# Performance work log

Hardware: AMD Instinct MI355X
Metric: run time of the kernel (lower is better)

Reference implementation:

```python
import jax, jax.numpy as jnp
import numpy as np

ROTARY_DIM = 32
THETA = 10000.0

def _rotate_half(t):
    # interleaved pairs: (..., d) -> rotate each (x1, x2) pair to (-x2, x1)
    x = t.reshape(t.shape[:-1] + (-1, 2))
    x1, x2 = x[..., 0], x[..., 1]
    return jnp.stack([-x2, x1], axis=-1).reshape(t.shape)

def _apply_rope(t, offset=0):
    # t: (B, h, T, dh); rotate only the first ROTARY_DIM dims
    T = t.shape[-2]
    inv_freq = 1.0 / (THETA ** (jnp.arange(0, ROTARY_DIM, 2, dtype=jnp.float32) / ROTARY_DIM))
    pos = jnp.arange(T, dtype=jnp.float32) + offset
    freqs = pos[:, None] * inv_freq[None, :]                 # (T, ROTARY_DIM/2)
    freqs = jnp.repeat(freqs, 2, axis=-1)                    # (T, ROTARY_DIM) interleaved
    cos, sin = jnp.cos(freqs), jnp.sin(freqs)
    t_rot, t_pass = t[..., :ROTARY_DIM], t[..., ROTARY_DIM:]
    t_rot = t_rot * cos + _rotate_half(t_rot) * sin
    return jnp.concatenate([t_rot, t_pass], axis=-1)

def setup_inputs() -> dict:
    key = jax.random.key(0)
    k1, k2, k3 = jax.random.split(key, 3)
    B, T, dim = 4, 1024, 1024
    x = jax.random.normal(k1, (B, T, dim), dtype=jnp.float32)
    Wqkv = jax.random.normal(k2, (dim, 3 * dim), dtype=jnp.float32) * (dim ** -0.5)
    Wout = jax.random.normal(k3, (dim, dim), dtype=jnp.float32) * (dim ** -0.5)
    return {"x": x, "Wqkv": Wqkv, "Wout": Wout}

def reference(x, Wqkv, Wout):
    B, T, dim = x.shape
    n_heads = 16
    dh = dim // n_heads
    qkv = x @ Wqkv                                            # (B, T, 3*dim)
    qkv = qkv.reshape(B, T, 3, n_heads, dh)
    qkv = jnp.transpose(qkv, (2, 0, 3, 1, 4))                 # (3, B, h, T, dh)
    q, k, v = qkv[0], qkv[1], qkv[2]
    q = _apply_rope(q, offset=0)
    k = _apply_rope(k, offset=0)
    scale = 1.0 / jnp.sqrt(jnp.asarray(dh, dtype=x.dtype))
    scores = jnp.einsum('bhqd,bhkd->bhqk', q, k) * scale      # (B, h, T, T)
    causal = jnp.tril(jnp.ones((T, T), dtype=bool))
    scores = jnp.where(causal, scores, jnp.asarray(-jnp.inf, dtype=scores.dtype))
    attn = jax.nn.softmax(scores, axis=-1)
    out = jnp.einsum('bhqk,bhkd->bhqd', attn, v)              # (B, h, T, dh)
    out = jnp.transpose(out, (0, 2, 1, 3)).reshape(B, T, dim)
    return out @ Wout
```

## Files before the change

kernel.cpp:

```cpp
#include <hip/hip_runtime.h>
#include <cstdint>
#include <cstddef>

typedef __bf16 bf16;
typedef __bf16 bf16x4 __attribute__((ext_vector_type(4)));
typedef __bf16 bf16x8 __attribute__((ext_vector_type(8)));
typedef float f32x4 __attribute__((ext_vector_type(4)));

#define DEVINL __device__ __forceinline__

static constexpr int Tn   = 1024;
static constexpr int DIM  = 1024;
static constexpr int NH   = 16;
static constexpr int DH   = 64;
static constexpr int QKVN = 3072;

DEVINL void g2l16(const void* g, void* l) {
  __builtin_amdgcn_global_load_lds(
      (const __attribute__((address_space(1))) void*)g,
      (__attribute__((address_space(3))) void*)l, 16, 0, 0);
}


__global__ void k_f32_to_bf16(const float* __restrict__ in, bf16* __restrict__ out, int n4) {
  int i = blockIdx.x * blockDim.x + threadIdx.x;
  if (i >= n4) return;
  float4 v = reinterpret_cast<const float4*>(in)[i];
  bf16 o[4] = {(bf16)v.x, (bf16)v.y, (bf16)v.z, (bf16)v.w};
  reinterpret_cast<uint2*>(out)[i] = *reinterpret_cast<uint2*>(o);
}

__global__ void k_transpose_w(const float* __restrict__ in, bf16* __restrict__ out, int K, int N) {
  __shared__ float tile[32][33];
  int n0 = blockIdx.x * 32, k0 = blockIdx.y * 32;
  int tx = threadIdx.x, ty = threadIdx.y;
#pragma unroll
  for (int j = 0; j < 32; j += 8)
    tile[ty + j][tx] = in[(size_t)(k0 + ty + j) * N + n0 + tx];
  __syncthreads();
#pragma unroll
  for (int j = 0; j < 32; j += 8)
    out[(size_t)(n0 + ty + j) * K + k0 + tx] = (bf16)tile[tx][ty + j];
}

__global__ void k_rope(bf16* __restrict__ qkv) {
  int idx = blockIdx.x * 256 + threadIdx.x;
  int i = idx & 15;
  int h = (idx >> 4) & 15;
  int w = (idx >> 8) & 1;
  int t = (idx >> 9) & 1023;
  int b = idx >> 19;
  float inv = exp2f(-(float)(2 * i) * (13.287712379549449f / 32.0f));
  float ang = (float)t * inv;
  float sn, cs;
  sincosf(ang, &sn, &cs);
  size_t base = ((size_t)(b * Tn + t)) * QKVN + (size_t)w * DIM + h * DH + 2 * i;
  float x1 = (float)qkv[base], x2 = (float)qkv[base + 1];
  qkv[base]     = (bf16)(x1 * cs - x2 * sn);
  qkv[base + 1] = (bf16)(x2 * cs + x1 * sn);
}

__global__ void k_transpose_v(const bf16* __restrict__ qkv, bf16* __restrict__ vt) {
  __shared__ bf16 tile[32][33];
  int t0 = blockIdx.x * 32, d0 = blockIdx.y * 32;
  int bh = blockIdx.z;
  int b = bh >> 4, h = bh & 15;
  int tx = threadIdx.x, ty = threadIdx.y;
#pragma unroll
  for (int j = 0; j < 32; j += 8)
    tile[ty + j][tx] = qkv[((size_t)(b * Tn + t0 + ty + j)) * QKVN + 2 * DIM + h * DH + d0 + tx];
  __syncthreads();
#pragma unroll
  for (int j = 0; j < 32; j += 8)
    vt[((size_t)(bh * DH + d0 + ty + j)) * Tn + t0 + tx] = tile[tx][ty + j];
}

template <bool F32OUT>
__global__ __launch_bounds__(256) void k_gemm_bt(
    const bf16* __restrict__ A, const bf16* __restrict__ Bt,
    void* __restrict__ Cp, int M, int N, int K) {
  __shared__ bf16 As[128 * 64];
  __shared__ bf16 Bs[128 * 64];
  const int tid  = threadIdx.x;
  const int wave = tid >> 6, lane = tid & 63;
  const int lrow = lane & 15, quad = lane >> 4;
  const int m0 = blockIdx.y * 128, n0 = blockIdx.x * 128;
  const int wm = (wave >> 1) * 64, wn = (wave & 1) * 64;

  f32x4 acc[4][4];
#pragma unroll
  for (int mi = 0; mi < 4; mi++)
#pragma unroll
    for (int ni = 0; ni < 4; ni++) acc[mi][ni] = 0.f;

  for (int k0 = 0; k0 < K; k0 += 64) {
    __syncthreads();
#pragma unroll
    for (int i = 0; i < 4; i++) {
      int li = i * 256 + tid;
      int row = li >> 3, c = li & 7;
      int gc = c ^ (row & 7);
      g2l16(A + (size_t)(m0 + row) * K + k0 + gc * 8, As + li * 8);
    }
#pragma unroll
    for (int i = 0; i < 4; i++) {
      int li = i * 256 + tid;
      int row = li >> 3, c = li & 7;
      int gc = c ^ (row & 7);
      g2l16(Bt + (size_t)(n0 + row) * K + k0 + gc * 8, Bs + li * 8);
    }
    __syncthreads();
#pragma unroll
    for (int ki = 0; ki < 2; ki++) {
      bf16x8 af[4], bfr[4];
#pragma unroll
      for (int mi = 0; mi < 4; mi++) {
        int r = wm + mi * 16 + lrow;
        int pc = (ki * 4 + quad) ^ (r & 7);
        af[mi] = *reinterpret_cast<const bf16x8*>(As + r * 64 + pc * 8);
      }
#pragma unroll
      for (int ni = 0; ni < 4; ni++) {
        int r = wn + ni * 16 + lrow;
        int pc = (ki * 4 + quad) ^ (r & 7);
        bfr[ni] = *reinterpret_cast<const bf16x8*>(Bs + r * 64 + pc * 8);
      }
#pragma unroll
      for (int mi = 0; mi < 4; mi++)
#pragma unroll
        for (int ni = 0; ni < 4; ni++)
          acc[mi][ni] = __builtin_amdgcn_mfma_f32_16x16x32_bf16(af[mi], bfr[ni], acc[mi][ni], 0, 0, 0);
    }
  }

#pragma unroll
  for (int mi = 0; mi < 4; mi++)
#pragma unroll
    for (int ni = 0; ni < 4; ni++) {
      int col = n0 + wn + ni * 16 + lrow;
#pragma unroll
      for (int r = 0; r < 4; r++) {
        int row = m0 + wm + mi * 16 + quad * 4 + r;
        float v = acc[mi][ni][r];
        if (F32OUT)
          reinterpret_cast<float*>(Cp)[(size_t)row * N + col] = v;
        else
          reinterpret_cast<bf16*>(Cp)[(size_t)row * N + col] = (bf16)v;
      }
    }
}

__global__ __launch_bounds__(256) void k_attn(
    const bf16* __restrict__ qkv, const bf16* __restrict__ vt,
    bf16* __restrict__ ao) {
  __shared__ bf16 Ks[2][64 * 64];
  __shared__ bf16 Vs[2][64 * 64];
  __shared__ bf16 Ps[8][16 * 64];

  const int tid  = threadIdx.x;
  const int wave = tid >> 6, lane = tid & 63;
  const int lrow = lane & 15, quad = lane >> 4;
  const int bh = blockIdx.y, b = bh >> 4, h = bh & 15;
  const int jn = blockIdx.x;
  const int jf = 15 - jn;
  const int qwf = jf * 64 + wave * 16;
  const int qwn = jn * 64 + wave * 16;
  const size_t qbase = (size_t)b * Tn * QKVN;

  bf16x8 qff[2], qfn[2];
  {
    const float SC = 0.125f * 1.44269504088896f;
    const bf16* qpf = qkv + qbase + (size_t)(qwf + lrow) * QKVN + h * DH;
    const bf16* qpn = qkv + qbase + (size_t)(qwn + lrow) * QKVN + h * DH;
    qff[0] = *reinterpret_cast<const bf16x8*>(qpf + quad * 8);
    qff[1] = *reinterpret_cast<const bf16x8*>(qpf + 32 + quad * 8);
    qfn[0] = *reinterpret_cast<const bf16x8*>(qpn + quad * 8);
    qfn[1] = *reinterpret_cast<const bf16x8*>(qpn + 32 + quad * 8);
#pragma unroll
    for (int j = 0; j < 8; j++) {
      qff[0][j] = (bf16)((float)qff[0][j] * SC);
      qff[1][j] = (bf16)((float)qff[1][j] * SC);
      qfn[0][j] = (bf16)((float)qfn[0][j] * SC);
      qfn[1][j] = (bf16)((float)qfn[1][j] * SC);
    }
  }

  f32x4 oaf[4], oan[4];
#pragma unroll
  for (int g = 0; g < 4; g++) { oaf[g] = 0.f; oan[g] = 0.f; }
  float lif = 0.f, lin = 0.f;

  const int ntiles = jf + 1;

  auto stage = [&](int k0, int bufi) {
#pragma unroll
    for (int i = 0; i < 2; i++) {
      int li2 = i * 256 + tid;
      int row = li2 >> 3, c = li2 & 7;
      int gc = c ^ (row & 7);
      g2l16(qkv + qbase + (size_t)(k0 + row) * QKVN + DIM + h * DH + gc * 8,
            &Ks[bufi][li2 * 8]);
      g2l16(vt + ((size_t)bh * DH + row) * Tn + k0 + gc * 8,
            &Vs[bufi][li2 * 8]);
    }
  };

  auto unit = [&](const bf16* ks, const bf16* vs, bf16x8 (&qf)[2], f32x4 (&oa)[4],
                  float& li, int pi, bool diag) {
    f32x4 s[4];
#pragma unroll
    for (int g = 0; g < 4; g++) s[g] = 0.f;
#pragma unroll
    for (int kh = 0; kh < 2; kh++) {
      const int cX = ((kh * 4 + quad) ^ (lrow & 7)) << 3;
#pragma unroll
      for (int g = 0; g < 4; g++) {
        bf16x8 kf = *reinterpret_cast<const bf16x8*>(ks + (g * 16 + lrow) * 64 + cX);
        s[g] = __builtin_amdgcn_mfma_f32_16x16x32_bf16(kf, qf[kh], s[g], 0, 0, 0);
      }
    }
    float psum = 0.f;
    const int qrel = wave * 16 + lrow;
#pragma unroll
    for (int g = 0; g < 4; g++) {
      bf16x4 pk;
#pragma unroll
      for (int r = 0; r < 4; r++) {
        float p = exp2f(s[g][r]);
        if (diag) {
          int kl = g * 16 + quad * 4 + r;
          p = (kl <= qrel) ? p : 0.f;
        }
        psum += p;
        pk[r] = (bf16)p;
      }
      int chunk = 2 * g + (quad >> 1);
      *reinterpret_cast<bf16x4*>(
          Ps[pi] + lrow * 64 + ((chunk ^ (lrow & 7)) << 3) + 4 * (quad & 1)) = pk;
    }
    li += psum;
#pragma unroll
    for (int kh = 0; kh < 2; kh++) {
      const int cX = ((kh * 4 + quad) ^ (lrow & 7)) << 3;
      bf16x8 pf = *reinterpret_cast<const bf16x8*>(Ps[pi] + lrow * 64 + cX);
#pragma unroll
      for (int g = 0; g < 4; g++) {
        bf16x8 vf = *reinterpret_cast<const bf16x8*>(vs + (g * 16 + lrow) * 64 + cX);
        oa[g] = __builtin_amdgcn_mfma_f32_16x16x32_bf16(pf, vf, oa[g], 0, 0, 0);
      }
    }
  };

  stage(0, 0);

  for (int kt = 0; kt < ntiles; kt++) {
    const int buf = kt & 1;
    __syncthreads();
    if (kt + 1 < ntiles) stage((kt + 1) << 6, buf ^ 1);

    const bf16* ks = Ks[buf];
    const bf16* vs = Vs[buf];

    unit(ks, vs, qff, oaf, lif, wave * 2 + 0, kt == jf);
    if (kt <= jn)
      unit(ks, vs, qfn, oan, lin, wave * 2 + 1, kt == jn);
  }

  lif += __shfl_xor(lif, 16, 64); lif += __shfl_xor(lif, 32, 64);
  lin += __shfl_xor(lin, 16, 64); lin += __shfl_xor(lin, 32, 64);

#pragma unroll
  for (int r = 0; r < 4; r++) {
    int m = quad * 4 + r;
    float invf = 1.0f / __shfl(lif, m, 64);
    float invn = 1.0f / __shfl(lin, m, 64);
    bf16* dstf = ao + ((size_t)b * Tn + qwf + m) * DIM + h * DH;
    bf16* dstn = ao + ((size_t)b * Tn + qwn + m) * DIM + h * DH;
    dstf[ 0 + lrow] = (bf16)(oaf[0][r] * invf);
    dstf[16 + lrow] = (bf16)(oaf[1][r] * invf);
    dstf[32 + lrow] = (bf16)(oaf[2][r] * invf);
    dstf[48 + lrow] = (bf16)(oaf[3][r] * invf);
    dstn[ 0 + lrow] = (bf16)(oan[0][r] * invn);
    dstn[16 + lrow] = (bf16)(oan[1][r] * invn);
    dstn[32 + lrow] = (bf16)(oan[2][r] * invn);
    dstn[48 + lrow] = (bf16)(oan[3][r] * invn);
  }
}

extern "C" void kernel_launch(void* const* d_in, const int* in_sizes, int n_in,
                              void* d_out, int out_size, void* d_ws, size_t ws_size,
                              hipStream_t stream) {
  const float* x    = (const float*)d_in[0];
  const float* Wqkv = (const float*)d_in[1];
  const float* Wout = (const float*)d_in[2];
  char* ws = (char*)d_ws;

  bf16* xb    = (bf16*)(ws + 0);
  bf16* wqkvT = (bf16*)(ws + 8388608);
  bf16* woutT = (bf16*)(ws + 14680064);
  bf16* qkv   = (bf16*)(ws + 16777216);
  bf16* vt    = (bf16*)(ws + 41943040);
  bf16* ao    = (bf16*)(ws + 50331648);

  k_f32_to_bf16<<<4096, 256, 0, stream>>>(x, xb, 1048576);
  k_transpose_w<<<dim3(96, 32), dim3(32, 8), 0, stream>>>(Wqkv, wqkvT, 1024, 3072);
  k_transpose_w<<<dim3(32, 32), dim3(32, 8), 0, stream>>>(Wout, woutT, 1024, 1024);
  k_gemm_bt<false><<<dim3(24, 32), 256, 0, stream>>>(xb, wqkvT, (void*)qkv, 4096, 3072, 1024);
  k_rope<<<8192, 256, 0, stream>>>(qkv);
  k_transpose_v<<<dim3(32, 2, 64), dim3(32, 8), 0, stream>>>(qkv, vt);
  k_attn<<<dim3(8, 64), 256, 0, stream>>>(qkv, vt, ao);
  k_gemm_bt<true><<<dim3(8, 32), 256, 0, stream>>>(ao, woutT, d_out, 4096, 1024, 1024);
  (void)in_sizes; (void)n_in; (void)out_size; (void)ws_size;
}
```

Measured before the change: 176.2 us.

## Fuse RoPE into QKV GEMM epilogue, narrow output GEMM tile, shrink attention P buffer

Removes the separate RoPE kernel by applying the rotation in the QKV GEMM epilogue, getting each pair partner through a lane shuffle and computing sin/cos per element. The output projection GEMM uses a 64-wide N tile, which doubles its block count and should improve occupancy across CUs. The attention kernel shares one P scratch buffer per wave, cutting LDS use. The cost is extra sincosf work in the GEMM epilogue and a less efficient, narrower tile in the output GEMM.

```diff
diff --git a/kernel.cpp b/kernel.cpp
--- a/kernel.cpp
+++ b/kernel.cpp
@@ -43,23 +43,6 @@
     out[(size_t)(n0 + ty + j) * K + k0 + tx] = (bf16)tile[tx][ty + j];
 }
 
-__global__ void k_rope(bf16* __restrict__ qkv) {
-  int idx = blockIdx.x * 256 + threadIdx.x;
-  int i = idx & 15;
-  int h = (idx >> 4) & 15;
-  int w = (idx >> 8) & 1;
-  int t = (idx >> 9) & 1023;
-  int b = idx >> 19;
-  float inv = exp2f(-(float)(2 * i) * (13.287712379549449f / 32.0f));
-  float ang = (float)t * inv;
-  float sn, cs;
-  sincosf(ang, &sn, &cs);
-  size_t base = ((size_t)(b * Tn + t)) * QKVN + (size_t)w * DIM + h * DH + 2 * i;
-  float x1 = (float)qkv[base], x2 = (float)qkv[base + 1];
-  qkv[base]     = (bf16)(x1 * cs - x2 * sn);
-  qkv[base + 1] = (bf16)(x2 * cs + x1 * sn);
-}
-
 __global__ void k_transpose_v(const bf16* __restrict__ qkv, bf16* __restrict__ vt) {
   __shared__ bf16 tile[32][33];
   int t0 = blockIdx.x * 32, d0 = blockIdx.y * 32;
@@ -75,23 +58,24 @@
     vt[((size_t)(bh * DH + d0 + ty + j)) * Tn + t0 + tx] = tile[tx][ty + j];
 }
 
-template <bool F32OUT>
+template <bool F32OUT, int BN, bool ROPE>
 __global__ __launch_bounds__(256) void k_gemm_bt(
     const bf16* __restrict__ A, const bf16* __restrict__ Bt,
     void* __restrict__ Cp, int M, int N, int K) {
+  constexpr int NI = BN / 32;
   __shared__ bf16 As[128 * 64];
-  __shared__ bf16 Bs[128 * 64];
+  __shared__ bf16 Bs[BN * 64];
   const int tid  = threadIdx.x;
   const int wave = tid >> 6, lane = tid & 63;
   const int lrow = lane & 15, quad = lane >> 4;
-  const int m0 = blockIdx.y * 128, n0 = blockIdx.x * 128;
-  const int wm = (wave >> 1) * 64, wn = (wave & 1) * 64;
-
-  f32x4 acc[4][4];
+  const int m0 = blockIdx.y * 128, n0 = blockIdx.x * BN;
+  const int wm = (wave >> 1) * 64, wn = (wave & 1) * (BN / 2);
+
+  f32x4 acc[4][NI];
 #pragma unroll
   for (int mi = 0; mi < 4; mi++)
 #pragma unroll
-    for (int ni = 0; ni < 4; ni++) acc[mi][ni] = 0.f;
+    for (int ni = 0; ni < NI; ni++) acc[mi][ni] = 0.f;
 
   for (int k0 = 0; k0 < K; k0 += 64) {
     __syncthreads();
@@ -103,7 +87,7 @@
       g2l16(A + (size_t)(m0 + row) * K + k0 + gc * 8, As + li * 8);
     }
 #pragma unroll
-    for (int i = 0; i < 4; i++) {
+    for (int i = 0; i < BN / 32; i++) {
       int li = i * 256 + tid;
       int row = li >> 3, c = li & 7;
       int gc = c ^ (row & 7);
@@ -112,7 +96,7 @@
     __syncthreads();
 #pragma unroll
     for (int ki = 0; ki < 2; ki++) {
-      bf16x8 af[4], bfr[4];
+      bf16x8 af[4], bfr[NI];
 #pragma unroll
       for (int mi = 0; mi < 4; mi++) {
         int r = wm + mi * 16 + lrow;
@@ -120,7 +104,7 @@
         af[mi] = *reinterpret_cast<const bf16x8*>(As + r * 64 + pc * 8);
       }
 #pragma unroll
-      for (int ni = 0; ni < 4; ni++) {
+      for (int ni = 0; ni < NI; ni++) {
         int r = wn + ni * 16 + lrow;
         int pc = (ki * 4 + quad) ^ (r & 7);
         bfr[ni] = *reinterpret_cast<const bf16x8*>(Bs + r * 64 + pc * 8);
@@ -128,7 +112,7 @@
 #pragma unroll
       for (int mi = 0; mi < 4; mi++)
 #pragma unroll
-        for (int ni = 0; ni < 4; ni++)
+        for (int ni = 0; ni < NI; ni++)
           acc[mi][ni] = __builtin_amdgcn_mfma_f32_16x16x32_bf16(af[mi], bfr[ni], acc[mi][ni], 0, 0, 0);
     }
   }
@@ -136,12 +120,26 @@
 #pragma unroll
   for (int mi = 0; mi < 4; mi++)
 #pragma unroll
-    for (int ni = 0; ni < 4; ni++) {
+    for (int ni = 0; ni < NI; ni++) {
       int col = n0 + wn + ni * 16 + lrow;
+      bool rot = false;
+      float inv = 0.f;
+      if (ROPE) {
+        rot = (col < 2 * DIM) && ((col & 63) < 32);
+        inv = exp2f(-(float)((col >> 1) & 15) * 0.830482023721841f);
+      }
 #pragma unroll
       for (int r = 0; r < 4; r++) {
         int row = m0 + wm + mi * 16 + quad * 4 + r;
         float v = acc[mi][ni][r];
+        if (ROPE) {
+          float pv = __shfl_xor(v, 1, 64);
+          if (rot) {
+            float sn, cs;
+            sincosf((float)(row & (Tn - 1)) * inv, &sn, &cs);
+            v = (col & 1) ? (v * cs + pv * sn) : (v * cs - pv * sn);
+          }
+        }
         if (F32OUT)
           reinterpret_cast<float*>(Cp)[(size_t)row * N + col] = v;
         else
@@ -155,7 +153,7 @@
     bf16* __restrict__ ao) {
   __shared__ bf16 Ks[2][64 * 64];
   __shared__ bf16 Vs[2][64 * 64];
-  __shared__ bf16 Ps[8][16 * 64];
+  __shared__ bf16 Ps[4][16 * 64];
 
   const int tid  = threadIdx.x;
   const int wave = tid >> 6, lane = tid & 63;
@@ -206,7 +204,7 @@
   };
 
   auto unit = [&](const bf16* ks, const bf16* vs, bf16x8 (&qf)[2], f32x4 (&oa)[4],
-                  float& li, int pi, bool diag) {
+                  float& li, bool diag) {
     f32x4 s[4];
 #pragma unroll
     for (int g = 0; g < 4; g++) s[g] = 0.f;
@@ -236,13 +234,13 @@
       }
       int chunk = 2 * g + (quad >> 1);
       *reinterpret_cast<bf16x4*>(
-          Ps[pi] + lrow * 64 + ((chunk ^ (lrow & 7)) << 3) + 4 * (quad & 1)) = pk;
+          Ps[wave] + lrow * 64 + ((chunk ^ (lrow & 7)) << 3) + 4 * (quad & 1)) = pk;
     }
     li += psum;
 #pragma unroll
     for (int kh = 0; kh < 2; kh++) {
       const int cX = ((kh * 4 + quad) ^ (lrow & 7)) << 3;
-      bf16x8 pf = *reinterpret_cast<const bf16x8*>(Ps[pi] + lrow * 64 + cX);
+      bf16x8 pf = *reinterpret_cast<const bf16x8*>(Ps[wave] + lrow * 64 + cX);
 #pragma unroll
       for (int g = 0; g < 4; g++) {
         bf16x8 vf = *reinterpret_cast<const bf16x8*>(vs + (g * 16 + lrow) * 64 + cX);
@@ -261,9 +259,9 @@
     const bf16* ks = Ks[buf];
     const bf16* vs = Vs[buf];
 
-    unit(ks, vs, qff, oaf, lif, wave * 2 + 0, kt == jf);
+    unit(ks, vs, qff, oaf, lif, kt == jf);
     if (kt <= jn)
-      unit(ks, vs, qfn, oan, lin, wave * 2 + 1, kt == jn);
+      unit(ks, vs, qfn, oan, lin, kt == jn);
   }
 
   lif += __shfl_xor(lif, 16, 64); lif += __shfl_xor(lif, 32, 64);
@@ -305,10 +303,11 @@
   k_f32_to_bf16<<<4096, 256, 0, stream>>>(x, xb, 1048576);
   k_transpose_w<<<dim3(96, 32), dim3(32, 8), 0, stream>>>(Wqkv, wqkvT, 1024, 3072);
   k_transpose_w<<<dim3(32, 32), dim3(32, 8), 0, stream>>>(Wout, woutT, 1024, 1024);
-  k_gemm_bt<false><<<dim3(24, 32), 256, 0, stream>>>(xb, wqkvT, (void*)qkv, 4096, 3072, 1024);
-  k_rope<<<8192, 256, 0, stream>>>(qkv);
+  k_gemm_bt<false, 128, true><<<dim3(24, 32), 256, 0, stream>>>(
+      xb, wqkvT, (void*)qkv, 4096, 3072, 1024);
   k_transpose_v<<<dim3(32, 2, 64), dim3(32, 8), 0, stream>>>(qkv, vt);
   k_attn<<<dim3(8, 64), 256, 0, stream>>>(qkv, vt, ao);
-  k_gemm_bt<true><<<dim3(8, 32), 256, 0, stream>>>(ao, woutT, d_out, 4096, 1024, 1024);
+  k_gemm_bt<true, 64, false><<<dim3(16, 32), 256, 0, stream>>>(
+      ao, woutT, d_out, 4096, 1024, 1024);
   (void)in_sizes; (void)n_in; (void)out_size; (void)ws_size;
 }
```

Result: slower. 182.3 us (+3.5%).
